# Kernel tuning notes

Hardware: AMD Instinct MI355X
Metric: run time of the kernel (lower is better)

## Reference

```python
import jax, jax.numpy as jnp
import numpy as np

T, N, C, S = 1600, 32, 512, 200
BLANK = 0
ALPHA = 0.5
NEG = -1e30  # finite stand-in for -inf (safe for grads)


def setup_inputs() -> dict:
    key = jax.random.key(0)
    k1, k2, k3 = jax.random.split(key, 3)
    # valid log-probabilities (log-softmax over vocab), shape (T, N, C)
    log_probs = jax.nn.log_softmax(jax.random.normal(k1, (T, N, C), jnp.float32), axis=-1)
    # labels in [1, C) so blank=0 never appears in targets
    targets = jax.random.randint(k2, (N, S), 1, C)
    input_lens = jnp.full((N,), T, dtype=jnp.int32)
    target_lens = jax.random.randint(k3, (N,), S // 2, S + 1)
    return {"log_probs": log_probs, "targets": targets,
            "input_lens": input_lens, "target_lens": target_lens}


def _ctc_forward(log_probs, targets, input_lens, target_lens):
    """Per-example CTC negative log-likelihood (reduction='none')."""
    Tt, Nn, Cc = log_probs.shape
    Ss = targets.shape[1]
    L = 2 * Ss + 1  # extended label sequence: blank, l1, blank, l2, ...

    ext = jnp.zeros((Nn, L), dtype=targets.dtype).at[:, 1::2].set(targets)  # (N, L)
    s_idx = jnp.arange(L)
    ext_m2 = jnp.pad(ext, ((0, 0), (2, 0)), constant_values=BLANK)[:, :L]
    # skip transition s-2 -> s allowed only for non-blank labels differing from s-2
    allow_skip = (ext != BLANK) & (ext != ext_m2) & (s_idx >= 2)[None, :]

    emit0 = jnp.take_along_axis(log_probs[0], ext, axis=1)  # (N, L)
    alpha0 = jnp.full((Nn, L), NEG, jnp.float32)
    alpha0 = alpha0.at[:, 0].set(emit0[:, 0])
    alpha0 = alpha0.at[:, 1].set(jnp.where(target_lens >= 1, emit0[:, 1], NEG))

    def step(alpha, xs):
        lp_t, t = xs  # lp_t: (N, C)
        emit = jnp.take_along_axis(lp_t, ext, axis=1)  # (N, L)
        a1 = jnp.pad(alpha, ((0, 0), (1, 0)), constant_values=NEG)[:, :L]
        a2 = jnp.where(allow_skip,
                       jnp.pad(alpha, ((0, 0), (2, 0)), constant_values=NEG)[:, :L],
                       NEG)
        m = jnp.maximum(jnp.maximum(alpha, a1), a2)
        new = m + jnp.log(jnp.exp(alpha - m) + jnp.exp(a1 - m) + jnp.exp(a2 - m)) + emit
        active = (t < input_lens)[:, None]  # freeze trellis past input_len
        return jnp.where(active, new, alpha), None

    alpha, _ = jax.lax.scan(step, alpha0, (log_probs[1:], jnp.arange(1, Tt)))

    idx_last = (2 * target_lens).astype(jnp.int32)  # final blank position
    idx_prev = jnp.maximum(idx_last - 1, 0)  # final label position
    a_last = jnp.take_along_axis(alpha, idx_last[:, None], axis=1)[:, 0]
    a_prev = jnp.where(target_lens > 0,
                       jnp.take_along_axis(alpha, idx_prev[:, None], axis=1)[:, 0],
                       NEG)
    return -jnp.logaddexp(a_last, a_prev)  # (N,)


def reference(log_probs, targets, input_lens, target_lens):
    per_ex = _ctc_forward(log_probs, targets, input_lens, target_lens)
    # zero_infinity=True: zero out infeasible alignments
    per_ex = jnp.where(per_ex < 1e29, per_ex, 0.0)
    norm = jnp.maximum(target_lens.astype(jnp.float32), 1.0) ** ALPHA
    return jnp.mean(per_ex / norm)
```

## Files before the change

### kernel.cpp

```cpp
#include <hip/hip_runtime.h>

#define T_DIM 1600
#define N_DIM 32
#define C_DIM 512
#define S_DIM 200
#define RCP_LN2 1.44269504088896340736f
#define LN2F 0.69314718055994530942f
#define ESENT (-(1 << 28))

static __device__ __forceinline__ float fast_exp2(float x) {
#if __has_builtin(__builtin_amdgcn_exp2f)
    return __builtin_amdgcn_exp2f(x);
#else
    return exp2f(x);
#endif
}

static __device__ __forceinline__ float fast_log2(float x) {
#if __has_builtin(__builtin_amdgcn_logf)
    return __builtin_amdgcn_logf(x);
#else
    return log2f(x);
#endif
}

static __device__ __forceinline__ float dpp_shr1_f(float x) {
    return __int_as_float(__builtin_amdgcn_update_dpp(
        0, __float_as_int(x), 0x138, 0xf, 0xf, false));
}
static __device__ __forceinline__ float dpp_shl1_f(float x) {
    return __int_as_float(__builtin_amdgcn_update_dpp(
        0, __float_as_int(x), 0x130, 0xf, 0xf, false));
}
static __device__ __forceinline__ int dpp_shr1_i(int x, int old0) {
    return __builtin_amdgcn_update_dpp(old0, x, 0x138, 0xf, 0xf, false);
}
static __device__ __forceinline__ int dpp_prefix_max_i(int x) {
    int t;
    t = __builtin_amdgcn_update_dpp(x, x, 0x111, 0xf, 0xf, false); x = (t > x) ? t : x;
    t = __builtin_amdgcn_update_dpp(x, x, 0x112, 0xf, 0xf, false); x = (t > x) ? t : x;
    t = __builtin_amdgcn_update_dpp(x, x, 0x114, 0xf, 0xf, false); x = (t > x) ? t : x;
    t = __builtin_amdgcn_update_dpp(x, x, 0x118, 0xf, 0xf, false); x = (t > x) ? t : x;
    t = __builtin_amdgcn_update_dpp(x, x, 0x142, 0xf, 0xf, false); x = (t > x) ? t : x;
    t = __builtin_amdgcn_update_dpp(x, x, 0x143, 0xf, 0xf, false); x = (t > x) ? t : x;
    return x;
}

static __device__ __forceinline__ void gl_lds16(const float* g, float* l) {
    __builtin_amdgcn_global_load_lds(
        (const __attribute__((address_space(1))) unsigned int*)g,
        (__attribute__((address_space(3))) unsigned int*)l, 16, 0, 0);
}

#define VMWAIT2()  __builtin_amdgcn_s_waitcnt(0x0F72)
#define VMWAIT8()  __builtin_amdgcn_s_waitcnt(0x0F78)
#define VMWAIT16() __builtin_amdgcn_s_waitcnt(0x4F70)
#define VMDRAIN()  __builtin_amdgcn_s_waitcnt(0x0F70)
#define SCHED0()   __builtin_amdgcn_sched_barrier(0)

#define WS_COUNT_F    64
#define WS_FIN_F      (N_DIM * 1152)
#define WS_PBL_OFF    (WS_COUNT_F + WS_FIN_F)
#define WS_PBL_F      (N_DIM * T_DIM + 256)
#define WS_PACKED_OFF (WS_PBL_OFF + WS_PBL_F)
#define WS_PACKED_F   ((size_t)N_DIM * T_DIM * 256)
#define WS_NEED_BYTES (((size_t)WS_PACKED_OFF + WS_PACKED_F) * 4)

__global__ __launch_bounds__(256) void ctc_pack(
    const float* __restrict__ lp, const int* __restrict__ tgts,
    float* __restrict__ packed, float* __restrict__ pblank)
{
    __shared__ float slab[4][2][C_DIM];

    const int wslot = threadIdx.x >> 6;
    const int lane = threadIdx.x & 63;
    const int wv = blockIdx.x * 4 + wslot;
    const int n = wv >> 7;
    const int w128 = wv & 127;
    const int* tgt = tgts + n * S_DIM;

    int l0 = 0, l1 = 0, l2 = 0, l3 = 0;
    if (lane < 50) {
        int4 li = reinterpret_cast<const int4*>(tgt)[lane];
        l0 = li.x; l1 = li.y; l2 = li.z; l3 = li.w;
    }
    if (l0 < 0 || l0 >= C_DIM) l0 = 0;
    if (l1 < 0 || l1 >= C_DIM) l1 = 0;
    if (l2 < 0 || l2 >= C_DIM) l2 = 0;
    if (l3 < 0 || l3 >= C_DIM) l3 = 0;

    float* sl0 = &slab[wslot][0][0];
    float* sl1 = &slab[wslot][1][0];
    const int nj = (T_DIM - 1 - w128) / 128 + 1;

    {
        const float* g = lp + ((size_t)w128 * N_DIM + n) * C_DIM + lane * 4;
        gl_lds16(g, sl0); gl_lds16(g + 256, sl0 + 256);
    }
    for (int j = 0; j < nj; ++j) {
        const int t = w128 + 128 * j;
        int tn = t + 128; if (tn >= T_DIM) tn = t;
        float* snx = (j & 1) ? sl0 : sl1;
        const float* gn = lp + ((size_t)tn * N_DIM + n) * C_DIM + lane * 4;
        gl_lds16(gn, snx); gl_lds16(gn + 256, snx + 256);
        VMWAIT2();
        SCHED0();
        const float* s = (j & 1) ? sl1 : sl0;
        float pb = s[0];
        float v0 = s[l0], v1 = s[l1], v2 = s[l2], v3 = s[l3];
        float4 o;
        o.x = fast_exp2(v0 * RCP_LN2);
        o.y = fast_exp2(v1 * RCP_LN2);
        o.z = fast_exp2(v2 * RCP_LN2);
        o.w = fast_exp2(v3 * RCP_LN2);
        reinterpret_cast<float4*>(packed)[((size_t)n * T_DIM + t) * 64 + lane] = o;
        if (lane == 0) pblank[n * T_DIM + t] = fast_exp2(pb * RCP_LN2);
    }
    VMDRAIN();
}

__global__ __launch_bounds__(64) void ctc_dp2(
    const int* __restrict__ tgts,
    const int* __restrict__ input_lens, const int* __restrict__ target_lens,
    const float* __restrict__ packed, const float* __restrict__ pblank,
    float* __restrict__ out, float* __restrict__ ws)
{
    __shared__ float pbl[1792];

    const int blk = blockIdx.x;
    const int n = blk >> 1;
    const int role = blk & 1;
    const int lane = threadIdx.x & 63;
    const int* tgt = tgts + n * S_DIM;

    int len = input_lens[n];
    if (len > T_DIM) len = T_DIM;
    const int lenc = (len < 1) ? 1 : len;
    const int tl = target_lens[n];
    const int mid = (lenc + 1) >> 1;
    const int nsb = lenc - mid;
    const int nsteps = (role == 0) ? mid : nsb;
    const int nc = (nsteps + 7) >> 3;
    const int ncx = ((nc + 1) >> 1) << 1;

    float* afin_g = ws + WS_COUNT_F + (size_t)n * 1152;
    float* bfin_g = afin_g + 512;
    int* escF_g = (int*)(afin_g + 1024);
    int* escB_g = escF_g + 64;
    int* counter = (int*)ws + n;

    float skh[4];
    if (role == 0) {
#pragma unroll
        for (int jj = 0; jj < 4; ++jj) {
            int s = lane * 8 + 2 * jj + 1;
            int i = (s - 1) >> 1;
            float al = 0.0f;
            if (i < S_DIM && s >= 3 && i >= 1)
                al = (tgt[i] != tgt[i - 1]) ? 1.0f : 0.0f;
            skh[jj] = al;
        }
    } else {
#pragma unroll
        for (int jj = 0; jj < 4; ++jj) {
            int shat = lane * 8 + 2 * jj + 1;
            int s = 510 - shat;
            float al = 0.0f;
            if (s >= 1 && s <= 399 && s + 2 <= 400)
                al = (tgt[(s + 1) >> 1] != tgt[(s - 1) >> 1]) ? 1.0f : 0.0f;
            skh[jj] = al;
        }
    }

    const int qlane = (role == 0) ? lane : (63 - lane);
    const float4* pk4 = reinterpret_cast<const float4*>(packed)
                        + (size_t)n * T_DIM * 64;

#pragma unroll
    for (int k = 0; k < 7; ++k)
        gl_lds16(pblank + (size_t)n * T_DIM + k * 256 + lane * 4, &pbl[k * 256]);
    VMDRAIN();
    SCHED0();

    auto tmap = [&](int ti) -> int {
        if (role == 0) return ti > mid - 1 ? mid - 1 : ti;
        int t = lenc - 1 - ti;
        return t < 0 ? 0 : t;
    };

#define LOADQ(QQ_, PQ_, c_) do {                                              \
        _Pragma("unroll")                                                     \
        for (int r_ = 0; r_ < 8; ++r_) {                                      \
            int t_ = tmap((c_) * 8 + r_);                                     \
            QQ_[r_] = pk4[(size_t)t_ * 64 + qlane];                           \
            PQ_[r_] = pbl[t_];                                                \
        }                                                                     \
    } while (0)

#define BOUNDARY() do {                                                       \
        float lm_ = fmaxf(fmaxf(fmaxf(a0, a1), fmaxf(a2, a3)),                \
                          fmaxf(fmaxf(a4, a5), fmaxf(a6, a7)));               \
        bool nz_ = (lm_ > 0.0f);                                              \
        int kl_ = (int)((__float_as_uint(lm_) >> 23) & 0xffu) - 127;          \
        int prop_ = nz_ ? (E + kl_) : ESENT;                                  \
        int g_ = dpp_prefix_max_i(prop_ + 32 * lane);                         \
        int Efin_ = g_ - 32 * lane;                                           \
        if (nz_) {                                                            \
            int sh_ = E - Efin_;                                              \
            int h1_ = sh_ / 2, h2_ = sh_ - h1_;                               \
            float f_ = fast_exp2((float)h1_), gg_ = fast_exp2((float)h2_);    \
            float fg_ = f_ * gg_;                                             \
            a0 *= fg_; a1 *= fg_; a2 *= fg_; a3 *= fg_;                       \
            a4 *= fg_; a5 *= fg_; a6 *= fg_; a7 *= fg_;                       \
        }                                                                     \
        int Eprev_ = dpp_shr1_i(Efin_, ESENT);                                \
        E = Efin_;                                                            \
        if (lane == 0) {                                                      \
            scale_d = 0.0f;                                                   \
        } else {                                                              \
            int d_ = Eprev_ - Efin_;                                          \
            scale_d = (d_ < -126) ? 0.0f : fast_exp2((float)d_);              \
        }                                                                     \
    } while (0)

#define COMPUTE_F2(c8_, FIRST_, QQ_, PQ_) do {                                \
        _Pragma("unroll")                                                     \
        for (int r_ = 0; r_ < 8; ++r_) {                                      \
            int t_ = (c8_) + r_;                                              \
            if (t_ >= mid) break;                                             \
            float pb_ = PQ_[r_];                                              \
            float p1_ = QQ_[r_].x, p3_ = QQ_[r_].y,                           \
                  p5_ = QQ_[r_].z, p7_ = QQ_[r_].w;                           \
            if ((FIRST_) && r_ == 0) {                                        \
                if (lane == 0) {                                              \
                    a0 = pb_;                                                 \
                    a1 = (tl >= 1) ? p1_ : 0.0f;                              \
                }                                                             \
            } else {                                                          \
                float P_ = dpp_shr1_f(a7) * scale_d;                          \
                float n0_ = (a0 + P_) * pb_;                                  \
                float n1_ = fmaf(skh[0], P_,  a1 + a0) * p1_;                 \
                float n2_ = (a2 + a1) * pb_;                                  \
                float n3_ = fmaf(skh[1], a1, a3 + a2) * p3_;                  \
                float n4_ = (a4 + a3) * pb_;                                  \
                float n5_ = fmaf(skh[2], a3, a5 + a4) * p5_;                  \
                float n6_ = (a6 + a5) * pb_;                                  \
                float n7_ = fmaf(skh[3], a5, a7 + a6) * p7_;                  \
                a0 = n0_; a1 = n1_; a2 = n2_; a3 = n3_;                       \
                a4 = n4_; a5 = n5_; a6 = n6_; a7 = n7_;                       \
            }                                                                 \
        }                                                                     \
    } while (0)

#define COMPUTE_B2(c8_, QQ_, PQ_) do {                                        \
        _Pragma("unroll")                                                     \
        for (int r_ = 0; r_ < 8; ++r_) {                                      \
            int ti_ = (c8_) + r_;                                             \
            if (ti_ >= nsb) break;                                            \
            float pb_ = PQ_[r_];                                              \
            float p1_ = QQ_[r_].z, p3_ = QQ_[r_].y, p5_ = QQ_[r_].x;          \
            float p7_ = dpp_shl1_f(QQ_[r_].w);                                \
            float c0_ = pb_ * a0, c1_ = p1_ * a1;                             \
            float c2_ = pb_ * a2, c3_ = p3_ * a3;                             \
            float c4_ = pb_ * a4, c5_ = p5_ * a5;                             \
            float c6_ = pb_ * a6, c7_ = p7_ * a7;                             \
            float P_ = dpp_shr1_f(c7_) * scale_d;                             \
            a0 = c0_ + P_;                                                    \
            a1 = fmaf(skh[0], P_,  c1_ + c0_);                                \
            a2 = c2_ + c1_;                                                   \
            a3 = fmaf(skh[1], c1_, c3_ + c2_);                                \
            a4 = c4_ + c3_;                                                   \
            a5 = fmaf(skh[2], c3_, c5_ + c4_);                                \
            a6 = c6_ + c5_;                                                   \
            a7 = fmaf(skh[3], c5_, c7_ + c6_);                                \
        }                                                                     \
    } while (0)

    float a0, a1, a2, a3, a4, a5, a6, a7;
    if (role == 0) {
        a0 = a1 = a2 = a3 = a4 = a5 = a6 = a7 = 0.0f;
    } else {
#define BINIT(aj_, j_) do {                                                   \
            int s_ = 510 - (lane * 8 + (j_));                                 \
            aj_ = (s_ == 2 * tl || (tl > 0 && s_ == 2 * tl - 1)) ? 1.0f : 0.0f; \
        } while (0)
        BINIT(a0, 0); BINIT(a1, 1); BINIT(a2, 2); BINIT(a3, 3);
        BINIT(a4, 4); BINIT(a5, 5); BINIT(a6, 6); BINIT(a7, 7);
#undef BINIT
    }
    int E = 0;
    float scale_d = (lane == 0) ? 0.0f : 1.0f;

    float4 qA[8], qB[8];
    float pbA[8], pbB[8];
    LOADQ(qA, pbA, 0);
    LOADQ(qB, pbB, 1);

    for (int k = 0; k < ncx; k += 2) {
        VMWAIT8();
        SCHED0();
        if (role == 0) { COMPUTE_F2(k * 8, (k == 0), qA, pbA); }
        else           { COMPUTE_B2(k * 8, qA, pbA); }
        BOUNDARY();
        LOADQ(qA, pbA, k + 2);
        VMWAIT8();
        SCHED0();
        if (role == 0) { COMPUTE_F2((k + 1) * 8, false, qB, pbB); }
        else           { COMPUTE_B2((k + 1) * 8, qB, pbB); }
        BOUNDARY();
        LOADQ(qB, pbB, k + 3);
    }
    VMDRAIN();

    {
        float4 lo = make_float4(a0, a1, a2, a3);
        float4 hi = make_float4(a4, a5, a6, a7);
        if (role == 0) {
            reinterpret_cast<float4*>(afin_g)[lane * 2] = lo;
            reinterpret_cast<float4*>(afin_g)[lane * 2 + 1] = hi;
            escF_g[lane] = E;
        } else {
            reinterpret_cast<float4*>(bfin_g)[lane * 2] = lo;
            reinterpret_cast<float4*>(bfin_g)[lane * 2 + 1] = hi;
            escB_g[lane] = E;
        }
    }

    __threadfence();
    int prev = 0;
    if (lane == 0)
        prev = __hip_atomic_fetch_add(counter, 1, __ATOMIC_ACQ_REL,
                                      __HIP_MEMORY_SCOPE_AGENT);
    prev = __shfl(prev, 0);
    if (prev != 1) return;
    __threadfence();

    {
        const int l = lane;
        const int Ef = escF_g[l];
        float m8 = -1e30f, s8 = 0.0f;
#pragma unroll
        for (int j = 0; j < 8; ++j) {
            int s = 8 * l + j;
            float x = -1e30f;
            if (s <= 400) {
                float af = afin_g[s];
                int shat = 510 - s;
                float bf = bfin_g[shat];
                if (af > 0.0f && bf > 0.0f)
                    x = fast_log2(af) + fast_log2(bf) + (float)(Ef + escB_g[shat >> 3]);
            }
            float m2 = fmaxf(m8, x);
            s8 = s8 * fast_exp2(m8 - m2) + fast_exp2(x - m2);
            m8 = m2;
        }
        float M = m8, V = s8;
#pragma unroll
        for (int off = 1; off < 64; off <<= 1) {
            float Mo = __shfl_xor(M, off);
            float Vo = __shfl_xor(V, off);
            float Mn = fmaxf(M, Mo);
            V = V * fast_exp2(M - Mn) + Vo * fast_exp2(Mo - Mn);
            M = Mn;
        }
        if (l == 0) {
            float X = M + fast_log2(V);
            float per_ex = -LN2F * X;
            if (!(per_ex < 1e29f)) per_ex = 0.0f;
            float tlf = (float)tl;
            if (tlf < 1.0f) tlf = 1.0f;
            atomicAdd(out, per_ex / sqrtf(tlf) * (1.0f / N_DIM));
        }
    }
#undef LOADQ
#undef BOUNDARY
#undef COMPUTE_F2
#undef COMPUTE_B2
}

__global__ __launch_bounds__(192) void ctc_dp_fb(
    const float* __restrict__ lp, const int* __restrict__ tgts,
    const int* __restrict__ input_lens, const int* __restrict__ target_lens,
    float* __restrict__ out, float* __restrict__ ws)
{
    __shared__ float rows[3][8][C_DIM];
    __shared__ float slab[2][5][8][64];

#define PHASE_SYNC() do {                                                     \
        __builtin_amdgcn_sched_barrier(0);                                    \
        __builtin_amdgcn_s_waitcnt(0xC07F);                                   \
        __builtin_amdgcn_s_barrier();                                         \
        __builtin_amdgcn_sched_barrier(0);                                    \
    } while (0)

    const int blk = blockIdx.x;
    const int n = blk >> 1;
    const int role = blk & 1;
    const int tid = threadIdx.x;
    const int wid = tid >> 6;
    const int lane = tid & 63;
    const int* tgt = tgts + n * S_DIM;

    int len = input_lens[n];
    if (len > T_DIM) len = T_DIM;
    const int lenc = (len < 1) ? 1 : len;
    const int tl = target_lens[n];
    const int mid = (lenc + 1) >> 1;
    const int nsb = lenc - mid;
    const int nsteps = (role == 0) ? mid : nsb;
    const int nc = (nsteps + 7) >> 3;

    float* afin_g = ws + 64 + (size_t)n * 1152;
    float* bfin_g = afin_g + 512;
    int* escF_g = (int*)(afin_g + 1024);
    int* escB_g = escF_g + 64;
    int* counter = (int*)ws + n;

    int lab[4];
    float skh[4];
    if (role == 0) {
#pragma unroll
        for (int jj = 0; jj < 4; ++jj) {
            int s = lane * 8 + 2 * jj + 1;
            int i = (s - 1) >> 1;
            int lb = 0;
            float al = 0.0f;
            if (i < S_DIM) {
                lb = tgt[i];
                if (s >= 3 && i >= 1) al = (tgt[i] != tgt[i - 1]) ? 1.0f : 0.0f;
            }
            if (lb < 0 || lb >= C_DIM) lb = 0;
            lab[jj] = lb;
            skh[jj] = al;
        }
    } else {
#pragma unroll
        for (int jj = 0; jj < 4; ++jj) {
            int shat = lane * 8 + 2 * jj + 1;
            int s = 510 - shat;
            int lb = 0;
            float al = 0.0f;
            if (s >= 1 && s <= 399) {
                lb = tgt[(s - 1) >> 1];
                if (s + 2 <= 400) al = (tgt[(s + 1) >> 1] != tgt[(s - 1) >> 1]) ? 1.0f : 0.0f;
            }
            if (lb < 0 || lb >= C_DIM) lb = 0;
            lab[jj] = lb;
            skh[jj] = al;
        }
    }

    const int r0 = (wid == 1) ? 0 : 4;
    auto tmap = [&](int ti) -> int {
        if (role == 0) return ti > mid - 1 ? mid - 1 : ti;
        int t = lenc - 1 - ti;
        return t < 0 ? 0 : t;
    };

#define STAGE(B_, c_) do {                                                    \
        _Pragma("unroll")                                                     \
        for (int rr_ = 0; rr_ < 4; ++rr_) {                                   \
            int r_ = r0 + rr_;                                                \
            int t_ = tmap((c_) * 8 + r_);                                     \
            const float* g_ = lp + ((size_t)t_ * N_DIM + n) * C_DIM + lane*4; \
            gl_lds16(g_,       &rows[(B_)][r_][0]);                           \
            gl_lds16(g_ + 256, &rows[(B_)][r_][256]);                         \
        }                                                                     \
    } while (0)

#define CONV(B_, S_) do {                                                     \
        float v_[20];                                                         \
        _Pragma("unroll")                                                     \
        for (int rr_ = 0; rr_ < 4; ++rr_) {                                   \
            int r_ = r0 + rr_;                                                \
            v_[rr_ * 5 + 0] = rows[(B_)][r_][0];                              \
            v_[rr_ * 5 + 1] = rows[(B_)][r_][lab[0]];                         \
            v_[rr_ * 5 + 2] = rows[(B_)][r_][lab[1]];                         \
            v_[rr_ * 5 + 3] = rows[(B_)][r_][lab[2]];                         \
            v_[rr_ * 5 + 4] = rows[(B_)][r_][lab[3]];                         \
        }                                                                     \
        __builtin_amdgcn_sched_barrier(0);                                    \
        _Pragma("unroll")                                                     \
        for (int rr_ = 0; rr_ < 4; ++rr_) {                                   \
            int r_ = r0 + rr_;                                                \
            _Pragma("unroll")                                                 \
            for (int j_ = 0; j_ < 5; ++j_)                                    \
                slab[(S_)][j_][r_][lane] =                                    \
                    fast_exp2(v_[rr_ * 5 + j_] * RCP_LN2);                    \
        }                                                                     \
    } while (0)

#define BOUNDARY() do {                                                       \
        float lm_ = fmaxf(fmaxf(fmaxf(a0, a1), fmaxf(a2, a3)),                \
                          fmaxf(fmaxf(a4, a5), fmaxf(a6, a7)));               \
        bool nz_ = (lm_ > 0.0f);                                              \
        int kl_ = (int)((__float_as_uint(lm_) >> 23) & 0xffu) - 127;          \
        int prop_ = nz_ ? (E + kl_) : ESENT;                                  \
        int g_ = dpp_prefix_max_i(prop_ + 32 * lane);                         \
        int Efin_ = g_ - 32 * lane;                                           \
        if (nz_) {                                                            \
            int sh_ = E - Efin_;                                              \
            int h1_ = sh_ / 2, h2_ = sh_ - h1_;                               \
            float f_ = fast_exp2((float)h1_), gg_ = fast_exp2((float)h2_);    \
            float fg_ = f_ * gg_;                                             \
            a0 *= fg_; a1 *= fg_; a2 *= fg_; a3 *= fg_;                       \
            a4 *= fg_; a5 *= fg_; a6 *= fg_; a7 *= fg_;                       \
        }                                                                     \
        int Eprev_ = dpp_shr1_i(Efin_, ESENT);                                \
        E = Efin_;                                                            \
        if (lane == 0) {                                                      \
            scale_d = 0.0f;                                                   \
        } else {                                                              \
            int d_ = Eprev_ - Efin_;                                          \
            scale_d = (d_ < -126) ? 0.0f : fast_exp2((float)d_);              \
        }                                                                     \
    } while (0)

#define CONSUME_F(c8_, S_, FIRST_) do {                                       \
        float q_[40];                                                         \
        _Pragma("unroll")                                                     \
        for (int r_ = 0; r_ < 8; ++r_)                                        \
            _Pragma("unroll")                                                 \
            for (int j_ = 0; j_ < 5; ++j_)                                    \
                q_[r_ * 5 + j_] = slab[(S_)][j_][r_][lane];                   \
        __builtin_amdgcn_sched_barrier(0);                                    \
        _Pragma("unroll")                                                     \
        for (int r_ = 0; r_ < 8; ++r_) {                                      \
            int t_ = (c8_) + r_;                                              \
            if (t_ >= mid) break;                                             \
            float pb_ = q_[r_ * 5 + 0];                                       \
            float p1_ = q_[r_ * 5 + 1];                                       \
            float p3_ = q_[r_ * 5 + 2];                                       \
            float p5_ = q_[r_ * 5 + 3];                                       \
            float p7_ = q_[r_ * 5 + 4];                                       \
            if ((FIRST_) && r_ == 0) {                                        \
                if (lane == 0) {                                              \
                    a0 = pb_;                                                 \
                    a1 = (tl >= 1) ? p1_ : 0.0f;                              \
                }                                                             \
            } else {                                                          \
                float P_ = dpp_shr1_f(a7) * scale_d;                          \
                float n0_ = (a0 + P_) * pb_;                                  \
                float n1_ = fmaf(skh[0], P_,  a1 + a0) * p1_;                 \
                float n2_ = (a2 + a1) * pb_;                                  \
                float n3_ = fmaf(skh[1], a1, a3 + a2) * p3_;                  \
                float n4_ = (a4 + a3) * pb_;                                  \
                float n5_ = fmaf(skh[2], a3, a5 + a4) * p5_;                  \
                float n6_ = (a6 + a5) * pb_;                                  \
                float n7_ = fmaf(skh[3], a5, a7 + a6) * p7_;                  \
                a0 = n0_; a1 = n1_; a2 = n2_; a3 = n3_;                       \
                a4 = n4_; a5 = n5_; a6 = n6_; a7 = n7_;                       \
            }                                                                 \
        }                                                                     \
    } while (0)

#define CONSUME_B(c8_, S_) do {                                               \
        float q_[40];                                                         \
        _Pragma("unroll")                                                     \
        for (int r_ = 0; r_ < 8; ++r_)                                        \
            _Pragma("unroll")                                                 \
            for (int j_ = 0; j_ < 5; ++j_)                                    \
                q_[r_ * 5 + j_] = slab[(S_)][j_][r_][lane];                   \
        __builtin_amdgcn_sched_barrier(0);                                    \
        _Pragma("unroll")                                                     \
        for (int r_ = 0; r_ < 8; ++r_) {                                      \
            int ti_ = (c8_) + r_;                                             \
            if (ti_ >= nsb) break;                                            \
            float pb_ = q_[r_ * 5 + 0];                                       \
            float p1_ = q_[r_ * 5 + 1];                                       \
            float p3_ = q_[r_ * 5 + 2];                                       \
            float p5_ = q_[r_ * 5 + 3];                                       \
            float p7_ = q_[r_ * 5 + 4];                                       \
            float c0_ = pb_ * a0, c1_ = p1_ * a1;                             \
            float c2_ = pb_ * a2, c3_ = p3_ * a3;                             \
            float c4_ = pb_ * a4, c5_ = p5_ * a5;                             \
            float c6_ = pb_ * a6, c7_ = p7_ * a7;                             \
            float P_ = dpp_shr1_f(c7_) * scale_d;                             \
            a0 = c0_ + P_;                                                    \
            a1 = fmaf(skh[0], P_,  c1_ + c0_);                                \
            a2 = c2_ + c1_;                                                   \
            a3 = fmaf(skh[1], c1_, c3_ + c2_);                                \
            a4 = c4_ + c3_;                                                   \
            a5 = fmaf(skh[2], c3_, c5_ + c4_);                                \
            a6 = c6_ + c5_;                                                   \
            a7 = fmaf(skh[3], c5_, c7_ + c6_);                                \
        }                                                                     \
    } while (0)

    if (wid >= 1) {
        STAGE(0, 0);
        STAGE(1, 1);
        VMWAIT8();
        CONV(0, 0);
        STAGE(2, 2);
    }
    PHASE_SYNC();

    float a0, a1, a2, a3, a4, a5, a6, a7;
    if (role == 0) {
        a0 = a1 = a2 = a3 = a4 = a5 = a6 = a7 = 0.0f;
    } else {
#define BINIT(aj_, j_) do {                                                   \
            int s_ = 510 - (lane * 8 + (j_));                                 \
            aj_ = (s_ == 2 * tl || (tl > 0 && s_ == 2 * tl - 1)) ? 1.0f : 0.0f; \
        } while (0)
        BINIT(a0, 0); BINIT(a1, 1); BINIT(a2, 2); BINIT(a3, 3);
        BINIT(a4, 4); BINIT(a5, 5); BINIT(a6, 6); BINIT(a7, 7);
#undef BINIT
    }
    int E = 0;
    float scale_d = (lane == 0) ? 0.0f : 1.0f;

    int bg = 1, bi = 0, sw = 1, sr = 0;
    for (int k = 0; k < nc; ++k) {
        if (wid >= 1) {
            VMWAIT8();
            CONV(bg, sw);
            STAGE(bi, k + 3);
        } else {
            if (role == 0) { CONSUME_F(k * 8, sr, (k == 0)); }
            else           { CONSUME_B(k * 8, sr); }
            BOUNDARY();
        }
        PHASE_SYNC();
        bg = (bg == 2) ? 0 : bg + 1;
        bi = (bi == 2) ? 0 : bi + 1;
        sw ^= 1;
        sr ^= 1;
    }

    if (wid >= 1) {
        VMDRAIN();
        return;
    }

    {
        float4 lo = make_float4(a0, a1, a2, a3);
        float4 hi = make_float4(a4, a5, a6, a7);
        if (role == 0) {
            reinterpret_cast<float4*>(afin_g)[lane * 2] = lo;
            reinterpret_cast<float4*>(afin_g)[lane * 2 + 1] = hi;
            escF_g[lane] = E;
        } else {
            reinterpret_cast<float4*>(bfin_g)[lane * 2] = lo;
            reinterpret_cast<float4*>(bfin_g)[lane * 2 + 1] = hi;
            escB_g[lane] = E;
        }
    }

    __threadfence();
    int prev = 0;
    if (lane == 0)
        prev = __hip_atomic_fetch_add(counter, 1, __ATOMIC_ACQ_REL,
                                      __HIP_MEMORY_SCOPE_AGENT);
    prev = __shfl(prev, 0);
    if (prev != 1) return;
    __threadfence();

    {
        const int l = lane;
        const int Ef = escF_g[l];
        float m8 = -1e30f, s8 = 0.0f;
#pragma unroll
        for (int j = 0; j < 8; ++j) {
            int s = 8 * l + j;
            float x = -1e30f;
            if (s <= 400) {
                float af = afin_g[s];
                int shat = 510 - s;
                float bf = bfin_g[shat];
                if (af > 0.0f && bf > 0.0f)
                    x = fast_log2(af) + fast_log2(bf) + (float)(Ef + escB_g[shat >> 3]);
            }
            float m2 = fmaxf(m8, x);
            s8 = s8 * fast_exp2(m8 - m2) + fast_exp2(x - m2);
            m8 = m2;
        }
        float M = m8, V = s8;
#pragma unroll
        for (int off = 1; off < 64; off <<= 1) {
            float Mo = __shfl_xor(M, off);
            float Vo = __shfl_xor(V, off);
            float Mn = fmaxf(M, Mo);
            V = V * fast_exp2(M - Mn) + Vo * fast_exp2(Mo - Mn);
            M = Mn;
        }
        if (l == 0) {
            float X = M + fast_log2(V);
            float per_ex = -LN2F * X;
            if (!(per_ex < 1e29f)) per_ex = 0.0f;
            float tlf = (float)tl;
            if (tlf < 1.0f) tlf = 1.0f;
            atomicAdd(out, per_ex / sqrtf(tlf) * (1.0f / N_DIM));
        }
    }
#undef STAGE
#undef CONV
#undef BOUNDARY
#undef CONSUME_F
#undef CONSUME_B
#undef PHASE_SYNC
}

extern "C" void kernel_launch(void* const* d_in, const int* in_sizes, int n_in,
                              void* d_out, int out_size, void* d_ws, size_t ws_size,
                              hipStream_t stream) {
    (void)in_sizes; (void)n_in;
    const float* lp   = (const float*)d_in[0];
    const int* tgts   = (const int*)d_in[1];
    const int* ilens  = (const int*)d_in[2];
    const int* tlens  = (const int*)d_in[3];

    hipMemsetAsync(d_out, 0, (size_t)out_size * sizeof(float), stream);
    hipMemsetAsync(d_ws, 0, N_DIM * sizeof(int), stream);

    if (ws_size >= WS_NEED_BYTES) {
        float* wsf = (float*)d_ws;
        ctc_pack<<<1024, 256, 0, stream>>>(lp, tgts,
                                           wsf + WS_PACKED_OFF, wsf + WS_PBL_OFF);
        ctc_dp2<<<2 * N_DIM, 64, 0, stream>>>(tgts, ilens, tlens,
                                              wsf + WS_PACKED_OFF, wsf + WS_PBL_OFF,
                                              (float*)d_out, wsf);
    } else {
        ctc_dp_fb<<<2 * N_DIM, 192, 0, stream>>>(lp, tgts, ilens, tlens,
                                                 (float*)d_out, (float*)d_ws);
    }
}
```

Baseline: 271.3 us.

## Stream packed emissions through LDS ring buffer and fold counter reset into pack

The DP kernel no longer loads packed emission probabilities straight into registers with a two-deep double buffer. It issues direct global-to-LDS loads into a four-slot ring, prefetching three chunks ahead, and reads each chunk from LDS just before computing on it. This deepens the prefetch pipeline and lowers register pressure, at the cost of extra LDS traffic and an LDS read on the critical step chain. It also moves the counter reset from a separate memset into the first block of the pack kernel, removing one launch.

```diff
diff --git a/kernel.cpp b/kernel.cpp
--- a/kernel.cpp
+++ b/kernel.cpp
@@ -68,9 +68,12 @@
 
 __global__ __launch_bounds__(256) void ctc_pack(
     const float* __restrict__ lp, const int* __restrict__ tgts,
-    float* __restrict__ packed, float* __restrict__ pblank)
+    float* __restrict__ packed, float* __restrict__ pblank,
+    int* __restrict__ counters)
 {
     __shared__ float slab[4][2][C_DIM];
+
+    if (blockIdx.x == 0 && threadIdx.x < N_DIM) counters[threadIdx.x] = 0;
 
     const int wslot = threadIdx.x >> 6;
     const int lane = threadIdx.x & 63;
@@ -125,6 +128,7 @@
     const float* __restrict__ packed, const float* __restrict__ pblank,
     float* __restrict__ out, float* __restrict__ ws)
 {
+    __shared__ float ring[4][8][256];
     __shared__ float pbl[1792];
 
     const int blk = blockIdx.x;
@@ -141,7 +145,6 @@
     const int nsb = lenc - mid;
     const int nsteps = (role == 0) ? mid : nsb;
     const int nc = (nsteps + 7) >> 3;
-    const int ncx = ((nc + 1) >> 1) << 1;
 
     float* afin_g = ws + WS_COUNT_F + (size_t)n * 1152;
     float* bfin_g = afin_g + 512;
@@ -173,14 +176,7 @@
     }
 
     const int qlane = (role == 0) ? lane : (63 - lane);
-    const float4* pk4 = reinterpret_cast<const float4*>(packed)
-                        + (size_t)n * T_DIM * 64;
-
-#pragma unroll
-    for (int k = 0; k < 7; ++k)
-        gl_lds16(pblank + (size_t)n * T_DIM + k * 256 + lane * 4, &pbl[k * 256]);
-    VMDRAIN();
-    SCHED0();
+    const float* pk = packed + (size_t)n * T_DIM * 256;
 
     auto tmap = [&](int ti) -> int {
         if (role == 0) return ti > mid - 1 ? mid - 1 : ti;
@@ -188,11 +184,22 @@
         return t < 0 ? 0 : t;
     };
 
-#define LOADQ(QQ_, PQ_, c_) do {                                              \
+#define ISSUE_RING(c_) do {                                                   \
+        int slot_ = (c_) & 3;                                                 \
         _Pragma("unroll")                                                     \
         for (int r_ = 0; r_ < 8; ++r_) {                                      \
             int t_ = tmap((c_) * 8 + r_);                                     \
-            QQ_[r_] = pk4[(size_t)t_ * 64 + qlane];                           \
+            gl_lds16(pk + (size_t)t_ * 256 + lane * 4, &ring[slot_][r_][0]);  \
+        }                                                                     \
+    } while (0)
+
+#define READQ(QQ_, PQ_, c_) do {                                              \
+        int slot_ = (c_) & 3;                                                 \
+        _Pragma("unroll")                                                     \
+        for (int r_ = 0; r_ < 8; ++r_) {                                      \
+            int t_ = tmap((c_) * 8 + r_);                                     \
+            QQ_[r_] = *reinterpret_cast<const float4*>(                       \
+                          &ring[slot_][r_][qlane * 4]);                       \
             PQ_[r_] = pbl[t_];                                                \
         }                                                                     \
     } while (0)
@@ -276,6 +283,13 @@
         }                                                                     \
     } while (0)
 
+#pragma unroll
+    for (int k7 = 0; k7 < 7; ++k7)
+        gl_lds16(pblank + (size_t)n * T_DIM + k7 * 256 + lane * 4, &pbl[k7 * 256]);
+    ISSUE_RING(0);
+    ISSUE_RING(1);
+    ISSUE_RING(2);
+
     float a0, a1, a2, a3, a4, a5, a6, a7;
     if (role == 0) {
         a0 = a1 = a2 = a3 = a4 = a5 = a6 = a7 = 0.0f;
@@ -291,24 +305,17 @@
     int E = 0;
     float scale_d = (lane == 0) ? 0.0f : 1.0f;
 
-    float4 qA[8], qB[8];
-    float pbA[8], pbB[8];
-    LOADQ(qA, pbA, 0);
-    LOADQ(qB, pbB, 1);
-
-    for (int k = 0; k < ncx; k += 2) {
-        VMWAIT8();
+    float4 qq[8];
+    float pq[8];
+    for (int k = 0; k < nc; ++k) {
+        VMWAIT16();
         SCHED0();
-        if (role == 0) { COMPUTE_F2(k * 8, (k == 0), qA, pbA); }
-        else           { COMPUTE_B2(k * 8, qA, pbA); }
+        READQ(qq, pq, k);
+        SCHED0();
+        if (role == 0) { COMPUTE_F2(k * 8, (k == 0), qq, pq); }
+        else           { COMPUTE_B2(k * 8, qq, pq); }
         BOUNDARY();
-        LOADQ(qA, pbA, k + 2);
-        VMWAIT8();
-        SCHED0();
-        if (role == 0) { COMPUTE_F2((k + 1) * 8, false, qB, pbB); }
-        else           { COMPUTE_B2((k + 1) * 8, qB, pbB); }
-        BOUNDARY();
-        LOADQ(qB, pbB, k + 3);
+        ISSUE_RING(k + 3);
     }
     VMDRAIN();
 
@@ -372,7 +379,8 @@
             atomicAdd(out, per_ex / sqrtf(tlf) * (1.0f / N_DIM));
         }
     }
-#undef LOADQ
+#undef ISSUE_RING
+#undef READQ
 #undef BOUNDARY
 #undef COMPUTE_F2
 #undef COMPUTE_B2
@@ -712,16 +720,17 @@
     const int* tlens  = (const int*)d_in[3];
 
     hipMemsetAsync(d_out, 0, (size_t)out_size * sizeof(float), stream);
-    hipMemsetAsync(d_ws, 0, N_DIM * sizeof(int), stream);
 
     if (ws_size >= WS_NEED_BYTES) {
         float* wsf = (float*)d_ws;
         ctc_pack<<<1024, 256, 0, stream>>>(lp, tgts,
-                                           wsf + WS_PACKED_OFF, wsf + WS_PBL_OFF);
+                                           wsf + WS_PACKED_OFF, wsf + WS_PBL_OFF,
+                                           (int*)d_ws);
         ctc_dp2<<<2 * N_DIM, 64, 0, stream>>>(tgts, ilens, tlens,
                                               wsf + WS_PACKED_OFF, wsf + WS_PBL_OFF,
                                               (float*)d_out, wsf);
     } else {
+        hipMemsetAsync(d_ws, 0, N_DIM * sizeof(int), stream);
         ctc_dp_fb<<<2 * N_DIM, 192, 0, stream>>>(lp, tgts, ilens, tlens,
                                                  (float*)d_out, (float*)d_ws);
     }
```

Result: slower. 291.7 us (+7.5%).
